# Optimization experiments

Hardware: AMD Instinct MI355X
Metric: run time of the kernel (lower is better)

The kernel has to match this reference:

```python
import jax, jax.numpy as jnp
import numpy as np

N = 50000
E = 800000
NODE_DIM = 128
EDGE_DIM = 64


def leaky_relu(x, slope=0.2):
    return jnp.where(x >= 0, x, slope * x)


def setup_inputs() -> dict:
    key = jax.random.key(0)
    ks = jax.random.split(key, 12)
    node_feats = jax.random.normal(ks[0], (N, NODE_DIM), dtype=jnp.float32)
    edge_index = jax.random.randint(ks[1], (2, E), 0, N, dtype=jnp.int64)
    edge_feats = jax.random.normal(ks[2], (E, EDGE_DIM), dtype=jnp.float32)
    # msg_mlp: Linear(node+edge -> node), LeakyReLU(0.2), Linear(node -> node)
    s1 = 1.0 / np.sqrt(NODE_DIM + EDGE_DIM)
    s2 = 1.0 / np.sqrt(NODE_DIM)
    s3 = 1.0 / np.sqrt(2 * NODE_DIM)
    msg_w1 = jax.random.uniform(ks[3], (NODE_DIM + EDGE_DIM, NODE_DIM), jnp.float32, -s1, s1)
    msg_b1 = jax.random.uniform(ks[4], (NODE_DIM,), jnp.float32, -s1, s1)
    msg_w2 = jax.random.uniform(ks[5], (NODE_DIM, NODE_DIM), jnp.float32, -s2, s2)
    msg_b2 = jax.random.uniform(ks[6], (NODE_DIM,), jnp.float32, -s2, s2)
    # update_mlp: Linear(2*node -> node), LeakyReLU(0.2), Linear(node -> node)
    upd_w1 = jax.random.uniform(ks[7], (2 * NODE_DIM, NODE_DIM), jnp.float32, -s3, s3)
    upd_b1 = jax.random.uniform(ks[8], (NODE_DIM,), jnp.float32, -s3, s3)
    upd_w2 = jax.random.uniform(ks[9], (NODE_DIM, NODE_DIM), jnp.float32, -s2, s2)
    upd_b2 = jax.random.uniform(ks[10], (NODE_DIM,), jnp.float32, -s2, s2)
    return {
        "node_feats": node_feats,
        "edge_feats": edge_feats,
        "msg_w1": msg_w1, "msg_b1": msg_b1, "msg_w2": msg_w2, "msg_b2": msg_b2,
        "upd_w1": upd_w1, "upd_b1": upd_b1, "upd_w2": upd_w2, "upd_b2": upd_b2,
        "edge_index": edge_index,
    }


def reference(node_feats, edge_feats, msg_w1, msg_b1, msg_w2, msg_b2,
              upd_w1, upd_b1, upd_w2, upd_b2, edge_index):
    src = edge_index[0]
    dst = edge_index[1]
    # gather neighbor features, concat with edge features: (E, node+edge)
    msg_input = jnp.concatenate([node_feats[dst], edge_feats], axis=1)
    h = leaky_relu(msg_input @ msg_w1 + msg_b1)
    messages = h @ msg_w2 + msg_b2                       # (E, node_dim)
    # scatter-add messages to source nodes
    aggregated = jax.ops.segment_sum(messages, src, num_segments=node_feats.shape[0])
    update_input = jnp.concatenate([node_feats, aggregated], axis=1)  # (N, 2*node_dim)
    h2 = leaky_relu(update_input @ upd_w1 + upd_b1)
    return h2 @ upd_w2 + upd_b2                          # (N, node_dim)
```

## Files before the change

### kernel.cpp

```cpp
#include <hip/hip_runtime.h>
#include <hip/hip_bf16.h>

#define NNODES 50000
#define NEDGES 800000
#define NDIM   128
#define EDIM   64
#define K1     192
#define K2     256
#define NB     196

#define KP1 200
#define KPA 136
#define KPU 264
#define MSTR 132

typedef __attribute__((ext_vector_type(8))) short bf16x8;
typedef __attribute__((ext_vector_type(4))) short bf16x4;
typedef __attribute__((ext_vector_type(4))) float f32x4;

__device__ inline short f2bf(float f) {
  union { float f; unsigned u; } v; v.f = f;
  unsigned r = v.u + 0x7FFFu + ((v.u >> 16) & 1u);
  return (short)(r >> 16);
}

__device__ inline bf16x4 pack4(float4 v) {
  bf16x4 p;
  p[0] = f2bf(v.x); p[1] = f2bf(v.y); p[2] = f2bf(v.z); p[3] = f2bf(v.w);
  return p;
}

__global__ __launch_bounds__(256) void wt_kernel(const float* __restrict__ w,
                                                 short* __restrict__ wt, int K) {
  int i = blockIdx.x * 256 + threadIdx.x;
  if (i < K * NDIM) {
    int k = i >> 7;
    int n = i & 127;
    wt[n * K + k] = f2bf(w[i]);
  }
}

__global__ __launch_bounds__(256) void hist_kernel(const int* __restrict__ eidx,
                                                   int* __restrict__ cnt) {
  int i = blockIdx.x * 256 + threadIdx.x;
  if (i < NEDGES) atomicAdd(&cnt[eidx[i]], 1);
}

__global__ __launch_bounds__(256) void scan_reduce_kernel(const int* __restrict__ cnt,
                                                          int* __restrict__ bsum) {
  __shared__ int sh[256];
  int tid = threadIdx.x;
  int i = blockIdx.x * 256 + tid;
  sh[tid] = (i < NNODES) ? cnt[i] : 0;
  __syncthreads();
#pragma unroll
  for (int off = 128; off > 0; off >>= 1) {
    if (tid < off) sh[tid] += sh[tid + off];
    __syncthreads();
  }
  if (tid == 0) bsum[blockIdx.x] = sh[0];
}

__global__ __launch_bounds__(256) void scan_top_kernel(const int* __restrict__ bsum,
                                                       int* __restrict__ bscan) {
  __shared__ int sh[256];
  int tid = threadIdx.x;
  int v = (tid < NB) ? bsum[tid] : 0;
  sh[tid] = v;
  __syncthreads();
#pragma unroll
  for (int off = 1; off < 256; off <<= 1) {
    int t = (tid >= off) ? sh[tid - off] : 0;
    __syncthreads();
    sh[tid] += t;
    __syncthreads();
  }
  bscan[tid] = sh[tid] - v;
}

__global__ __launch_bounds__(256) void scan_down_kernel(int* __restrict__ cnt,
                                                        const int* __restrict__ bscan,
                                                        int* __restrict__ row_ptr) {
  __shared__ int sh[256];
  int tid = threadIdx.x;
  int i = blockIdx.x * 256 + tid;
  int v = (i < NNODES) ? cnt[i] : 0;
  sh[tid] = v;
  __syncthreads();
#pragma unroll
  for (int off = 1; off < 256; off <<= 1) {
    int t = (tid >= off) ? sh[tid - off] : 0;
    __syncthreads();
    sh[tid] += t;
    __syncthreads();
  }
  if (i < NNODES) {
    row_ptr[i] = bscan[blockIdx.x] + (sh[tid] - v);
    cnt[i] = 0;
  }
}

__global__ __launch_bounds__(256) void permute_kernel(const int* __restrict__ eidx,
                                                      const int* __restrict__ row_ptr,
                                                      int* __restrict__ cnt,
                                                      int4* __restrict__ s_edges) {
  int e = blockIdx.x * 256 + threadIdx.x;
  if (e < NEDGES) {
    int s = eidx[e];
    int d = eidx[NEDGES + e];
    int pos = row_ptr[s] + atomicAdd(&cnt[s], 1);
    s_edges[pos] = make_int4(s, d, e, 0);
  }
}

__global__ __launch_bounds__(256) void edge_kernel(const float* __restrict__ node_feats,
                                                   const float* __restrict__ edge_feats,
                                                   const int4* __restrict__ s_edges,
                                                   const short* __restrict__ w1t,
                                                   const float* __restrict__ b1,
                                                   float* __restrict__ hagg) {
  __shared__ __align__(16) char SH[64 * MSTR * 4];
  __shared__ int srcs[64];
  __shared__ int dsts[64];
  __shared__ int eids[64];

  short* X = (short*)SH;
  float* M = (float*)SH;

  const int tid = threadIdx.x;
  const int e0 = blockIdx.x * 64;

  if (tid < 64) {
    int4 v = s_edges[e0 + tid];
    srcs[tid] = v.x;
    dsts[tid] = v.y;
    eids[tid] = v.z;
  }
  __syncthreads();

  {
    int r = tid >> 2, q = tid & 3;
    const float4* np = (const float4*)(node_feats + (size_t)dsts[r] * NDIM) + q * 8;
    const float4* ep = (const float4*)(edge_feats + (size_t)eids[r] * EDIM) + q * 4;
    short* dpn = X + r * KP1 + q * 32;
    short* dpe = X + r * KP1 + NDIM + q * 16;
#pragma unroll
    for (int j = 0; j < 8; ++j) *(bf16x4*)(dpn + j * 4) = pack4(np[j]);
#pragma unroll
    for (int j = 0; j < 4; ++j) *(bf16x4*)(dpe + j * 4) = pack4(ep[j]);
  }
  __syncthreads();

  const int lane = tid & 63;
  const int wv = tid >> 6;
  const int m16 = lane & 15;
  const int quad = lane >> 4;

  f32x4 acc[4][2];
#pragma unroll
  for (int mt = 0; mt < 4; ++mt)
#pragma unroll
    for (int nt = 0; nt < 2; ++nt)
      acc[mt][nt] = (f32x4){0.f, 0.f, 0.f, 0.f};

#pragma unroll
  for (int ks = 0; ks < 6; ++ks) {
    const int k0 = ks * 32 + quad * 8;
    bf16x8 b[2];
#pragma unroll
    for (int nt = 0; nt < 2; ++nt) {
      int n = wv * 32 + nt * 16 + m16;
      b[nt] = *(const bf16x8*)(w1t + n * K1 + k0);
    }
#pragma unroll
    for (int mt = 0; mt < 4; ++mt) {
      bf16x8 a = *(const bf16x8*)(X + (mt * 16 + m16) * KP1 + k0);
#pragma unroll
      for (int nt = 0; nt < 2; ++nt)
        acc[mt][nt] = __builtin_amdgcn_mfma_f32_16x16x32_bf16(a, b[nt], acc[mt][nt], 0, 0, 0);
    }
  }
  __syncthreads();

#pragma unroll
  for (int nt = 0; nt < 2; ++nt) {
    int col = wv * 32 + nt * 16 + m16;
    float bias = b1[col];
#pragma unroll
    for (int mt = 0; mt < 4; ++mt) {
#pragma unroll
      for (int i = 0; i < 4; ++i) {
        float v = acc[mt][nt][i] + bias;
        v = v >= 0.f ? v : 0.2f * v;
        int row = mt * 16 + quad * 4 + i;
        M[row * MSTR + col] = v;
      }
    }
  }
  __syncthreads();

  if (tid < 128) {
    const int c = tid;
    float a = M[c];
    int prev = srcs[0];
#pragma unroll 4
    for (int r = 1; r < 64; ++r) {
      int s = srcs[r];
      float v = M[r * MSTR + c];
      if (s != prev) {
        atomicAdd(&hagg[(size_t)prev * NDIM + c], a);
        a = v;
        prev = s;
      } else {
        a += v;
      }
    }
    atomicAdd(&hagg[(size_t)prev * NDIM + c], a);
  }
}

__global__ __launch_bounds__(256) void node_kernel(const float* __restrict__ node_feats,
                                                   const float* __restrict__ hagg,
                                                   const int* __restrict__ degc,
                                                   const short* __restrict__ w2t,
                                                   const float* __restrict__ b2,
                                                   const short* __restrict__ u1t,
                                                   const float* __restrict__ ub1,
                                                   const short* __restrict__ u2t,
                                                   const float* __restrict__ ub2,
                                                   float* __restrict__ out) {
  __shared__ __align__(16) short AGH[64 * KPA];
  __shared__ __align__(16) short XU[64 * KPU];
  __shared__ float degs[64];

  const int tid = threadIdx.x;
  const int n0 = blockIdx.x * 64;

  if (tid < 64) {
    int node = n0 + tid;
    degs[tid] = (node < NNODES) ? (float)degc[node] : 0.f;
  }
  {
    int r = tid >> 2, q = tid & 3;
    int node = n0 + r; if (node >= NNODES) node = NNODES - 1;
    const float4* hp = (const float4*)(hagg + (size_t)node * NDIM) + q * 8;
    const float4* xp = (const float4*)(node_feats + (size_t)node * NDIM) + q * 8;
    short* ap = AGH + r * KPA + q * 32;
    short* xq = XU + r * KPU + q * 32;
#pragma unroll
    for (int j = 0; j < 8; ++j) {
      *(bf16x4*)(ap + j * 4) = pack4(hp[j]);
      *(bf16x4*)(xq + j * 4) = pack4(xp[j]);
    }
  }
  __syncthreads();

  const int lane = tid & 63;
  const int wv = tid >> 6;
  const int m16 = lane & 15;
  const int quad = lane >> 4;

  f32x4 acc[4][2];

#pragma unroll
  for (int mt = 0; mt < 4; ++mt)
#pragma unroll
    for (int nt = 0; nt < 2; ++nt)
      acc[mt][nt] = (f32x4){0.f, 0.f, 0.f, 0.f};
#pragma unroll
  for (int ks = 0; ks < 4; ++ks) {
    const int k0 = ks * 32 + quad * 8;
    bf16x8 b[2];
#pragma unroll
    for (int nt = 0; nt < 2; ++nt) {
      int n = wv * 32 + nt * 16 + m16;
      b[nt] = *(const bf16x8*)(w2t + n * NDIM + k0);
    }
#pragma unroll
    for (int mt = 0; mt < 4; ++mt) {
      bf16x8 a = *(const bf16x8*)(AGH + (mt * 16 + m16) * KPA + k0);
#pragma unroll
      for (int nt = 0; nt < 2; ++nt)
        acc[mt][nt] = __builtin_amdgcn_mfma_f32_16x16x32_bf16(a, b[nt], acc[mt][nt], 0, 0, 0);
    }
  }
#pragma unroll
  for (int nt = 0; nt < 2; ++nt) {
    int col = wv * 32 + nt * 16 + m16;
    float bb = b2[col];
#pragma unroll
    for (int mt = 0; mt < 4; ++mt) {
#pragma unroll
      for (int i = 0; i < 4; ++i) {
        int row = mt * 16 + quad * 4 + i;
        float v = acc[mt][nt][i] + degs[row] * bb;
        XU[row * KPU + NDIM + col] = f2bf(v);
      }
    }
  }
  __syncthreads();

#pragma unroll
  for (int mt = 0; mt < 4; ++mt)
#pragma unroll
    for (int nt = 0; nt < 2; ++nt)
      acc[mt][nt] = (f32x4){0.f, 0.f, 0.f, 0.f};
#pragma unroll
  for (int ks = 0; ks < 8; ++ks) {
    const int k0 = ks * 32 + quad * 8;
    bf16x8 b[2];
#pragma unroll
    for (int nt = 0; nt < 2; ++nt) {
      int n = wv * 32 + nt * 16 + m16;
      b[nt] = *(const bf16x8*)(u1t + n * K2 + k0);
    }
#pragma unroll
    for (int mt = 0; mt < 4; ++mt) {
      bf16x8 a = *(const bf16x8*)(XU + (mt * 16 + m16) * KPU + k0);
#pragma unroll
      for (int nt = 0; nt < 2; ++nt)
        acc[mt][nt] = __builtin_amdgcn_mfma_f32_16x16x32_bf16(a, b[nt], acc[mt][nt], 0, 0, 0);
    }
  }
  __syncthreads();
#pragma unroll
  for (int nt = 0; nt < 2; ++nt) {
    int col = wv * 32 + nt * 16 + m16;
    float bb = ub1[col];
#pragma unroll
    for (int mt = 0; mt < 4; ++mt) {
#pragma unroll
      for (int i = 0; i < 4; ++i) {
        int row = mt * 16 + quad * 4 + i;
        float v = acc[mt][nt][i] + bb;
        v = v >= 0.f ? v : 0.2f * v;
        AGH[row * KPA + col] = f2bf(v);
      }
    }
  }
  __syncthreads();

#pragma unroll
  for (int mt = 0; mt < 4; ++mt)
#pragma unroll
    for (int nt = 0; nt < 2; ++nt)
      acc[mt][nt] = (f32x4){0.f, 0.f, 0.f, 0.f};
#pragma unroll
  for (int ks = 0; ks < 4; ++ks) {
    const int k0 = ks * 32 + quad * 8;
    bf16x8 b[2];
#pragma unroll
    for (int nt = 0; nt < 2; ++nt) {
      int n = wv * 32 + nt * 16 + m16;
      b[nt] = *(const bf16x8*)(u2t + n * NDIM + k0);
    }
#pragma unroll
    for (int mt = 0; mt < 4; ++mt) {
      bf16x8 a = *(const bf16x8*)(AGH + (mt * 16 + m16) * KPA + k0);
#pragma unroll
      for (int nt = 0; nt < 2; ++nt)
        acc[mt][nt] = __builtin_amdgcn_mfma_f32_16x16x32_bf16(a, b[nt], acc[mt][nt], 0, 0, 0);
    }
  }
#pragma unroll
  for (int nt = 0; nt < 2; ++nt) {
    int col = wv * 32 + nt * 16 + m16;
    float bb = ub2[col];
#pragma unroll
    for (int mt = 0; mt < 4; ++mt) {
#pragma unroll
      for (int i = 0; i < 4; ++i) {
        int row = mt * 16 + quad * 4 + i;
        int node = n0 + row;
        if (node < NNODES)
          out[(size_t)node * NDIM + col] = acc[mt][nt][i] + bb;
      }
    }
  }
}

extern "C" void kernel_launch(void* const* d_in, const int* in_sizes, int n_in,
                              void* d_out, int out_size, void* d_ws, size_t ws_size,
                              hipStream_t stream) {
  const float* node_feats = (const float*)d_in[0];
  const float* edge_feats = (const float*)d_in[1];
  const float* msg_w1 = (const float*)d_in[2];
  const float* msg_b1 = (const float*)d_in[3];
  const float* msg_w2 = (const float*)d_in[4];
  const float* msg_b2 = (const float*)d_in[5];
  const float* upd_w1 = (const float*)d_in[6];
  const float* upd_b1 = (const float*)d_in[7];
  const float* upd_w2 = (const float*)d_in[8];
  const float* upd_b2 = (const float*)d_in[9];
  const int* eidx = (const int*)d_in[10];

  float* hagg   = (float*)d_ws;
  int* cnt      = (int*)(hagg + (size_t)NNODES * NDIM);
  int* row_ptr  = cnt + NNODES;
  int* bsum     = row_ptr + NNODES;
  int* bscan    = bsum + 256;
  int4* s_edges = (int4*)(bscan + 256);
  short* w1t    = (short*)(s_edges + NEDGES);
  short* w2t    = w1t + 128 * K1;
  short* u1t    = w2t + 128 * 128;
  short* u2t    = u1t + 128 * K2;

  hipMemsetAsync(d_ws, 0, (size_t)(NNODES * NDIM + NNODES) * sizeof(float), stream);

  wt_kernel<<<(K1 * 128) / 256, 256, 0, stream>>>(msg_w1, w1t, K1);
  wt_kernel<<<(128 * 128) / 256, 256, 0, stream>>>(msg_w2, w2t, 128);
  wt_kernel<<<(K2 * 128) / 256, 256, 0, stream>>>(upd_w1, u1t, K2);
  wt_kernel<<<(128 * 128) / 256, 256, 0, stream>>>(upd_w2, u2t, 128);

  hist_kernel<<<NEDGES / 256, 256, 0, stream>>>(eidx, cnt);
  scan_reduce_kernel<<<NB, 256, 0, stream>>>(cnt, bsum);
  scan_top_kernel<<<1, 256, 0, stream>>>(bsum, bscan);
  scan_down_kernel<<<NB, 256, 0, stream>>>(cnt, bscan, row_ptr);
  permute_kernel<<<NEDGES / 256, 256, 0, stream>>>(eidx, row_ptr, cnt, s_edges);

  edge_kernel<<<NEDGES / 64, 256, 0, stream>>>(node_feats, edge_feats, s_edges,
                                               w1t, msg_b1, hagg);
  node_kernel<<<(NNODES + 63) / 64, 256, 0, stream>>>(node_feats, hagg, cnt,
                                                      w2t, msg_b2, u1t, upd_b1,
                                                      u2t, upd_b2, (float*)d_out);
}
```

Baseline: 564.6 us.

## Pre-convert node features to bf16 and shrink edge kernel shared memory

A new kernel converts node features to bf16 once, so the edge kernel's random gather of destination rows reads half the bytes and skips per-edge conversion. The node kernel reads the same bf16 copy. The edge kernel's shared buffer drops to the bf16 tile size. The epilogue is split into two halves of 32 rows each, with all 256 threads doing segmented reductions over 16 rows, and launch bounds request 6 blocks per CU for higher occupancy. The cost is an extra conversion pass over node features and more atomics, because the run-length segments are shorter.

```diff
diff --git a/kernel.cpp b/kernel.cpp
--- a/kernel.cpp
+++ b/kernel.cpp
@@ -28,6 +28,15 @@
   bf16x4 p;
   p[0] = f2bf(v.x); p[1] = f2bf(v.y); p[2] = f2bf(v.z); p[3] = f2bf(v.w);
   return p;
+}
+
+__global__ __launch_bounds__(256) void cvt_kernel(const float* __restrict__ src,
+                                                  short* __restrict__ dst, int n) {
+  int i = (blockIdx.x * 256 + threadIdx.x) * 4;
+  if (i < n) {
+    float4 v = *(const float4*)(src + i);
+    *(bf16x4*)(dst + i) = pack4(v);
+  }
 }
 
 __global__ __launch_bounds__(256) void wt_kernel(const float* __restrict__ w,
@@ -113,13 +122,13 @@
   }
 }
 
-__global__ __launch_bounds__(256) void edge_kernel(const float* __restrict__ node_feats,
-                                                   const float* __restrict__ edge_feats,
-                                                   const int4* __restrict__ s_edges,
-                                                   const short* __restrict__ w1t,
-                                                   const float* __restrict__ b1,
-                                                   float* __restrict__ hagg) {
-  __shared__ __align__(16) char SH[64 * MSTR * 4];
+__global__ __launch_bounds__(256, 6) void edge_kernel(const short* __restrict__ nf_bf,
+                                                      const float* __restrict__ edge_feats,
+                                                      const int4* __restrict__ s_edges,
+                                                      const short* __restrict__ w1t,
+                                                      const float* __restrict__ b1,
+                                                      float* __restrict__ hagg) {
+  __shared__ __align__(16) char SH[64 * KP1 * 2];
   __shared__ int srcs[64];
   __shared__ int dsts[64];
   __shared__ int eids[64];
@@ -140,12 +149,12 @@
 
   {
     int r = tid >> 2, q = tid & 3;
-    const float4* np = (const float4*)(node_feats + (size_t)dsts[r] * NDIM) + q * 8;
+    const bf16x8* np = (const bf16x8*)(nf_bf + (size_t)dsts[r] * NDIM) + q * 4;
     const float4* ep = (const float4*)(edge_feats + (size_t)eids[r] * EDIM) + q * 4;
     short* dpn = X + r * KP1 + q * 32;
     short* dpe = X + r * KP1 + NDIM + q * 16;
 #pragma unroll
-    for (int j = 0; j < 8; ++j) *(bf16x4*)(dpn + j * 4) = pack4(np[j]);
+    for (int j = 0; j < 4; ++j) *(bf16x8*)(dpn + j * 8) = np[j];
 #pragma unroll
     for (int j = 0; j < 4; ++j) *(bf16x4*)(dpe + j * 4) = pack4(ep[j]);
   }
@@ -183,43 +192,49 @@
   __syncthreads();
 
 #pragma unroll
-  for (int nt = 0; nt < 2; ++nt) {
-    int col = wv * 32 + nt * 16 + m16;
-    float bias = b1[col];
-#pragma unroll
-    for (int mt = 0; mt < 4; ++mt) {
-#pragma unroll
-      for (int i = 0; i < 4; ++i) {
-        float v = acc[mt][nt][i] + bias;
-        v = v >= 0.f ? v : 0.2f * v;
-        int row = mt * 16 + quad * 4 + i;
-        M[row * MSTR + col] = v;
+  for (int h = 0; h < 2; ++h) {
+#pragma unroll
+    for (int nt = 0; nt < 2; ++nt) {
+      int col = wv * 32 + nt * 16 + m16;
+      float bb = b1[col];
+#pragma unroll
+      for (int mt2 = 0; mt2 < 2; ++mt2) {
+        int mt = h * 2 + mt2;
+#pragma unroll
+        for (int i = 0; i < 4; ++i) {
+          float v = acc[mt][nt][i] + bb;
+          v = v >= 0.f ? v : 0.2f * v;
+          int lr = mt2 * 16 + quad * 4 + i;
+          M[lr * MSTR + col] = v;
+        }
       }
     }
-  }
-  __syncthreads();
-
-  if (tid < 128) {
-    const int c = tid;
-    float a = M[c];
-    int prev = srcs[0];
+    __syncthreads();
+    {
+      const int c = tid & 127;
+      const int lr0 = (tid >> 7) * 16;
+      const int g0 = h * 32 + lr0;
+      float a = M[lr0 * MSTR + c];
+      int prev = srcs[g0];
 #pragma unroll 4
-    for (int r = 1; r < 64; ++r) {
-      int s = srcs[r];
-      float v = M[r * MSTR + c];
-      if (s != prev) {
-        atomicAdd(&hagg[(size_t)prev * NDIM + c], a);
-        a = v;
-        prev = s;
-      } else {
-        a += v;
+      for (int r = 1; r < 16; ++r) {
+        int s = srcs[g0 + r];
+        float v = M[(lr0 + r) * MSTR + c];
+        if (s != prev) {
+          atomicAdd(&hagg[(size_t)prev * NDIM + c], a);
+          a = v;
+          prev = s;
+        } else {
+          a += v;
+        }
       }
-    }
-    atomicAdd(&hagg[(size_t)prev * NDIM + c], a);
-  }
-}
-
-__global__ __launch_bounds__(256) void node_kernel(const float* __restrict__ node_feats,
+      atomicAdd(&hagg[(size_t)prev * NDIM + c], a);
+    }
+    if (h == 0) __syncthreads();
+  }
+}
+
+__global__ __launch_bounds__(256) void node_kernel(const short* __restrict__ nf_bf,
                                                    const float* __restrict__ hagg,
                                                    const int* __restrict__ degc,
                                                    const short* __restrict__ w2t,
@@ -244,14 +259,13 @@
     int r = tid >> 2, q = tid & 3;
     int node = n0 + r; if (node >= NNODES) node = NNODES - 1;
     const float4* hp = (const float4*)(hagg + (size_t)node * NDIM) + q * 8;
-    const float4* xp = (const float4*)(node_feats + (size_t)node * NDIM) + q * 8;
+    const bf16x8* xp = (const bf16x8*)(nf_bf + (size_t)node * NDIM) + q * 4;
     short* ap = AGH + r * KPA + q * 32;
     short* xq = XU + r * KPU + q * 32;
 #pragma unroll
-    for (int j = 0; j < 8; ++j) {
-      *(bf16x4*)(ap + j * 4) = pack4(hp[j]);
-      *(bf16x4*)(xq + j * 4) = pack4(xp[j]);
-    }
+    for (int j = 0; j < 8; ++j) *(bf16x4*)(ap + j * 4) = pack4(hp[j]);
+#pragma unroll
+    for (int j = 0; j < 4; ++j) *(bf16x8*)(xq + j * 8) = xp[j];
   }
   __syncthreads();
 
@@ -404,9 +418,12 @@
   short* w2t    = w1t + 128 * K1;
   short* u1t    = w2t + 128 * 128;
   short* u2t    = u1t + 128 * K2;
+  short* nf_bf  = u2t + 128 * 128;
 
   hipMemsetAsync(d_ws, 0, (size_t)(NNODES * NDIM + NNODES) * sizeof(float), stream);
 
+  cvt_kernel<<<(NNODES * NDIM / 4 + 255) / 256, 256, 0, stream>>>(node_feats, nf_bf,
+                                                                  NNODES * NDIM);
   wt_kernel<<<(K1 * 128) / 256, 256, 0, stream>>>(msg_w1, w1t, K1);
   wt_kernel<<<(128 * 128) / 256, 256, 0, stream>>>(msg_w2, w2t, 128);
   wt_kernel<<<(K2 * 128) / 256, 256, 0, stream>>>(upd_w1, u1t, K2);
@@ -418,9 +435,9 @@
   scan_down_kernel<<<NB, 256, 0, stream>>>(cnt, bscan, row_ptr);
   permute_kernel<<<NEDGES / 256, 256, 0, stream>>>(eidx, row_ptr, cnt, s_edges);
 
-  edge_kernel<<<NEDGES / 64, 256, 0, stream>>>(node_feats, edge_feats, s_edges,
+  edge_kernel<<<NEDGES / 64, 256, 0, stream>>>(nf_bf, edge_feats, s_edges,
                                                w1t, msg_b1, hagg);
-  node_kernel<<<(NNODES + 63) / 64, 256, 0, stream>>>(node_feats, hagg, cnt,
+  node_kernel<<<(NNODES + 63) / 64, 256, 0, stream>>>(nf_bf, hagg, cnt,
                                                       w2t, msg_b2, u1t, upd_b1,
                                                       u2t, upd_b2, (float*)d_out);
 }
```

New measurement: 541.1 us. -4.2%, faster.
